# Kernel tuning notes

Measured on AMD Instinct MI355X. Metric: run time of the kernel, lower is better.

Reference implementation:

```python
import jax, jax.numpy as jnp
import numpy as np

B = 32768
NPG = 15            # nodes per graph (5 segments * 3 nodes)
NSEG = 5
FEAT = 8
HID = 64
BIAS_SP = float(np.log(np.exp(1.0) - 1.0))  # biased_softplus_1.0 bias
SCALE_LB = 1e-4


def _edge_template():
    eg = []
    for s in range(NSEG):
        t = 3 * s
        eg += [(t, t + 1), (t + 1, t), (t, t + 2), (t + 2, t)]
    for s in range(NSEG - 1):
        eg += [(3 * s, 3 * s + 3), (3 * s + 3, 3 * s)]
    return np.asarray(eg, dtype=np.int64)  # [28, 2]


def setup_inputs() -> dict:
    key = jax.random.key(0)
    ks = jax.random.split(key, 16)
    N = B * NPG
    x = jax.random.normal(ks[0], (N, FEAT), dtype=jnp.float32)
    tmpl = _edge_template()
    offs = (np.arange(B, dtype=np.int64) * NPG)[:, None]          # [B,1]
    src = (tmpl[:, 0][None, :] + offs).ravel()
    dst = (tmpl[:, 1][None, :] + offs).ravel()
    edge_index = jnp.asarray(np.stack([src, dst]), dtype=jnp.int32)  # [2,E]
    sd = 0.05
    params = dict(
        Wt=jax.random.normal(ks[1], (FEAT, HID), jnp.float32) * sd,
        bt=jax.random.normal(ks[2], (HID,), jnp.float32) * sd,
        Wl=jax.random.normal(ks[3], (4, HID), jnp.float32) * sd,
        bl=jax.random.normal(ks[4], (HID,), jnp.float32) * sd,
        gc_Wroot=jax.random.normal(ks[5], (3, HID, HID), jnp.float32) * sd,
        gc_Wrel=jax.random.normal(ks[6], (3, HID, HID), jnp.float32) * sd,
        gc_b=jax.random.normal(ks[7], (3, HID), jnp.float32) * sd,
        leg_W=jax.random.normal(ks[8], (10, HID, 4), jnp.float32) * sd,
        leg_b=jax.random.normal(ks[9], (10, 4), jnp.float32) * sd,
        torso_W=jax.random.normal(ks[10], (4, HID, 4), jnp.float32) * sd,
        torso_b=jax.random.normal(ks[11], (4, 4), jnp.float32) * sd,
    )
    return dict(x=x, edge_index=edge_index, batch_size=B, **params)


def reference(x, edge_index, batch_size, Wt, bt, Wl, bl,
              gc_Wroot, gc_Wrel, gc_b, leg_W, leg_b, torso_W, torso_b):
    N = x.shape[0]
    npg = N // batch_size              # 15
    nseg = npg // 3                    # 5
    pos = jnp.arange(N) % npg
    is_torso = (pos % 3) == 0          # nodes 0,3,6,... within each graph

    # Per-type input encoders + tanh, merged by mask (original scatters into h)
    h_t = jnp.tanh(x @ Wt + bt)
    h_l = jnp.tanh(x[:, :4] @ Wl + bl)
    h = jnp.where(is_torso[:, None], h_t, h_l)        # [N, 64]

    src, dst = edge_index[0], edge_index[1]
    for i in range(3):
        agg = jax.ops.segment_sum(h[src], dst, num_segments=N)
        h = jnp.tanh(agg @ gc_Wrel[i] + gc_b[i] + h @ gc_Wroot[i])

    hp = h.reshape(batch_size, npg, HID)              # [B, 15, 64]

    leg_pos = jnp.array([p for p in range(1, npg) if p % 3 != 0])   # 10 legs
    torso_pos = jnp.array([3 * s for s in range(1, nseg)])          # 4 torsos

    leg_out = jnp.einsum('bnd,ndk->bnk', hp[:, leg_pos], leg_W) + leg_b      # [B,10,4]
    torso_out = jnp.einsum('bnd,ndk->bnk', hp[:, torso_pos], torso_W) + torso_b  # [B,4,4]

    # Blocks are emitted in node-position order 1..14 within each graph
    blocks = jnp.zeros((batch_size, npg - 1, 4), dtype=h.dtype)
    blocks = blocks.at[:, leg_pos - 1].set(leg_out)
    blocks = blocks.at[:, torso_pos - 1].set(torso_out)
    out = blocks.reshape(batch_size, 2 * (npg - 1), 2)               # [B,28,2]

    loc = out[..., 0]
    scale = jnp.maximum(jax.nn.softplus(out[..., 1] + BIAS_SP), SCALE_LB)
    return loc, scale
```

## Files before the change

### kernel.cpp

```cpp
#include <hip/hip_runtime.h>

#define NB 32768
#define GPB 8
#define THREADS 256
#define BIAS_SP 0.5413248546129181f

typedef __attribute__((ext_vector_type(8))) short bf16x8;
typedef __attribute__((ext_vector_type(4))) float f32x4;
typedef __attribute__((ext_vector_type(4))) unsigned int u32x4;

static __device__ __forceinline__ unsigned f2bfu(float f) {
    union { float f; unsigned u; } v; v.f = f;
    return (v.u + 0x8000u) >> 16;
}
static __device__ __forceinline__ float lof(unsigned u) {
    union { unsigned u; float f; } v; v.u = u << 16; return v.f;
}
static __device__ __forceinline__ float hif(unsigned u) {
    union { unsigned u; float f; } v; v.u = u & 0xFFFF0000u; return v.f;
}
static __device__ __forceinline__ float fast_tanh(float xx) {
    float e = __expf(2.0f * xx);
    return 1.0f - 2.0f * __builtin_amdgcn_rcpf(e + 1.0f);
}
#define CVTPK(d, a, b) asm("v_cvt_pk_bf16_f32 %0, %1, %2" : "=v"(d) : "v"(a), "v"(b))

__global__ void setup_kernel(const float* __restrict__ Wroot, const float* __restrict__ Wrel,
                             const float* __restrict__ legW, const float* __restrict__ torW,
                             const float* __restrict__ Wt, const float* __restrict__ bt,
                             const float* __restrict__ Wl, const float* __restrict__ bl,
                             unsigned* __restrict__ wsw) {
    const int t = blockIdx.x * 256 + threadIdx.x;
    if (t < 3072) {
        const int i = t >> 10, rem = t & 1023, s = rem >> 8, tt = rem & 255;
        const int lane = tt & 63, ctl = tt >> 6;
        const int bcol = (ctl << 4) + (lane & 15);
        const int kb = ((s & 1) << 5) + ((lane >> 4) << 3);
        const float* M = ((s < 2) ? Wroot : Wrel) + i * 4096 + kb * 64 + bcol;
        u32x4 d;
        #pragma unroll
        for (int dd = 0; dd < 4; ++dd)
            d[dd] = f2bfu(M[(2 * dd) * 64]) | (f2bfu(M[(2 * dd + 1) * 64]) << 16);
        *(u32x4*)(wsw + t * 4) = d;
    } else if (t < 3520) {
        const int t2 = t - 3072, item = t2 >> 3, k8 = t2 & 7;
        const int p = (item >> 2) + 1, j = item & 3;
        const int p3 = (p * 11) >> 5;
        const int pm3 = p - p3 * 3;
        const float* src;
        if (pm3 == 0) src = torW + (p3 - 1) * 256 + j;
        else          src = legW + (2 * p3 + pm3 - 1) * 256 + j;
        u32x4 d;
        #pragma unroll
        for (int dd = 0; dd < 4; ++dd) {
            const int k = (k8 << 3) + 2 * dd;
            d[dd] = f2bfu(src[k * 4]) | (f2bfu(src[(k + 1) * 4]) << 16);
        }
        *(u32x4*)(wsw + 12288 + t2 * 4) = d;
    } else if (t < 3776) {
        const int t3 = t - 3520;
        const int lane = t3 & 63, ctl = t3 >> 6;
        const int col = (ctl << 4) + (lane & 15);
        const int kg = lane >> 4;
        auto encval = [&](int k) -> float {
            if (k < 8)   return Wt[k * 64 + col];
            if (k < 12)  return Wl[(k - 8) * 64 + col];
            if (k == 12) return bt[col];
            if (k == 13) return bl[col];
            return 0.f;
        };
        u32x4 d;
        #pragma unroll
        for (int dd = 0; dd < 4; ++dd) {
            const int k0 = kg * 8 + 2 * dd;
            d[dd] = f2bfu(encval(k0)) | (f2bfu(encval(k0 + 1)) << 16);
        }
        *(u32x4*)(wsw + 14080 + t3 * 4) = d;
    }
}

__global__ __launch_bounds__(THREADS, 4) void leg_main(
    const float* __restrict__ x,
    const float* __restrict__ gcb,
    const float* __restrict__ legB, const float* __restrict__ torB,
    const unsigned* __restrict__ wsw,
    float* __restrict__ out)
{
    __shared__ __align__(16) unsigned char smem[GPB * 4096];
    const int tid  = threadIdx.x;
    const int lane = tid & 63;
    const int ct   = tid >> 6;
    const int g0   = blockIdx.x * GPB;

    const int bcol = (ct << 4) + (lane & 15);
    const float cb0 = gcb[bcol], cb1 = gcb[64 + bcol], cb2 = gcb[128 + bcol];

    const int row = lane & 15, kg = lane >> 4;
    const int row3 = (row * 11) >> 5;
    const int tors = row3 * 3;
    const int isT  = (row == tors);
    const int rowR = isT ? row : tors;
    const int voffA0  = row * 256 + (((kg ^ row) & 7) << 4);
    const int voffA1  = voffA0 ^ 0x40;
    const int voffA2  = rowR * 256 + (((kg ^ rowR) & 7) << 4) + (isT ? 128 : 0);
    const int voffA3  = voffA2 ^ 0x40;
    int voffC[4];
    #pragma unroll
    for (int r = 0; r < 4; ++r) {
        const int rr = (kg << 2) + r;
        voffC[r] = rr * 256 + (((((ct << 1) + ((lane >> 3) & 1)) ^ rr) & 7) << 4) + ((lane & 7) << 1);
    }

    const int c2 = lane & 31;
    unsigned char* gbase = smem + ((ct << 1) + (lane >> 5)) * 4096;
    const int aoff = (c2 & 3) << 2;
    int agg_ra[15];
    #pragma unroll
    for (int r = 0; r < 15; ++r)
        agg_ra[r] = r * 256 + ((((c2 >> 2) ^ r) & 7) << 4) + aoff;
    int agg_wa[5];
    #pragma unroll
    for (int i = 0; i < 5; ++i) {
        const int r = 3 * i;
        agg_wa[i] = r * 256 + 128 + ((((c2 >> 2) ^ r) & 7) << 4) + aoff;
    }
#define RD32(r)  (*(const unsigned*)(gbase + agg_ra[r]))
#define WR32(i, flo, fhi) do { unsigned _w; CVTPK(_w, flo, fhi); \
    *(unsigned*)(gbase + agg_wa[i]) = _w; } while (0)
#define AGG() do { \
    unsigned u[15]; \
    _Pragma("unroll") for (int r = 0; r < 15; ++r) u[r] = RD32(r); \
    float l3 = lof(u[3]), h3 = hif(u[3]), l6 = lof(u[6]), h6 = hif(u[6]), l9 = lof(u[9]), h9 = hif(u[9]); \
    WR32(0,  lof(u[1]) + lof(u[2]) + l3,              hif(u[1]) + hif(u[2]) + h3); \
    WR32(1,  lof(u[4]) + lof(u[5]) + lof(u[0]) + l6,  hif(u[4]) + hif(u[5]) + hif(u[0]) + h6); \
    WR32(2,  lof(u[7]) + lof(u[8]) + l3 + l9,         hif(u[7]) + hif(u[8]) + h3 + h9); \
    WR32(3,  lof(u[10]) + lof(u[11]) + l6 + lof(u[12]), hif(u[10]) + hif(u[11]) + h6 + hif(u[12])); \
    WR32(4,  lof(u[13]) + lof(u[14]) + l9,            hif(u[13]) + hif(u[14]) + h9); \
} while (0)
#define EPI() do { \
    _Pragma("unroll") for (int g = 0; g < GPB; ++g) { \
        _Pragma("unroll") for (int r = 0; r < 4; ++r) { \
            const float tv = fast_tanh(acc[g][r]); \
            unsigned uu; CVTPK(uu, tv, tv); \
            *(unsigned short*)(smem + g * 4096 + voffC[r]) = (unsigned short)uu; \
        } } } while (0)

    const unsigned mT = (isT && row < 15) ? 0xFFFFFFFFu : 0u;
    const unsigned mL = isT ? 0u : 0xFFFFFFFFu;
    const unsigned m01 = (kg == 0) ? mT : ((kg == 1) ? mL : 0u);
    const unsigned m45 = (kg == 0) ? mT : 0u;
    const unsigned c1213 = (kg == 1) ? ((mT ? 0x3F80u : 0u) | (mL ? 0x3F800000u : 0u)) : 0u;
    const int rowc = (row < 15) ? row : 0;
    const bf16x8 bfrE = *(const bf16x8*)(wsw + 14080 + tid * 4);

    f32x4 acc[GPB];
    #pragma unroll
    for (int g = 0; g < GPB; ++g) {
        const float4* xr = (const float4*)x + ((size_t)(g0 + g) * 15 + rowc) * 2;
        const float4 x0 = xr[0], x1 = xr[1];
        unsigned a01, a23, a45, a67;
        CVTPK(a01, x0.x, x0.y); CVTPK(a23, x0.z, x0.w);
        CVTPK(a45, x1.x, x1.y); CVTPK(a67, x1.z, x1.w);
        union { u32x4 u; bf16x8 b; } af;
        af.u[0] = a01 & m01;
        af.u[1] = a23 & m01;
        af.u[2] = (a45 & m45) | c1213;
        af.u[3] = a67 & m45;
        const f32x4 z = { 0.f, 0.f, 0.f, 0.f };
        acc[g] = __builtin_amdgcn_mfma_f32_16x16x32_bf16(af.b, bfrE, z, 0, 0, 0);
    }
    EPI();
    __syncthreads();
    AGG();
    __syncthreads();

    #pragma unroll
    for (int it = 0; it < 3; ++it) {
        bf16x8 bfr[4];
        #pragma unroll
        for (int s = 0; s < 4; ++s)
            bfr[s] = *(const bf16x8*)(wsw + ((it * 4 + s) * 256 + tid) * 4);
        const float cbi = (it == 0) ? cb0 : (it == 1) ? cb1 : cb2;
        #pragma unroll
        for (int g = 0; g < GPB; ++g) {
            const unsigned char* sg = smem + g * 4096;
            const bf16x8 a0 = *(const bf16x8*)(sg + voffA0);
            const bf16x8 a1 = *(const bf16x8*)(sg + voffA1);
            const bf16x8 a2 = *(const bf16x8*)(sg + voffA2);
            const bf16x8 a3 = *(const bf16x8*)(sg + voffA3);
            f32x4 c = { cbi, cbi, cbi, cbi };
            c = __builtin_amdgcn_mfma_f32_16x16x32_bf16(a0, bfr[0], c, 0, 0, 0);
            c = __builtin_amdgcn_mfma_f32_16x16x32_bf16(a1, bfr[1], c, 0, 0, 0);
            c = __builtin_amdgcn_mfma_f32_16x16x32_bf16(a2, bfr[2], c, 0, 0, 0);
            c = __builtin_amdgcn_mfma_f32_16x16x32_bf16(a3, bfr[3], c, 0, 0, 0);
            acc[g] = c;
        }
        __syncthreads();
        EPI();
        __syncthreads();
        if (it < 2) { AGG(); __syncthreads(); }
    }

    if (lane < 56) {
        const int p = (lane >> 2) + 1, j = lane & 3;
        const int p3 = (p * 11) >> 5;
        const int pm3 = p - p3 * 3;
        float bias;
        if (pm3 == 0) bias = torB[((p3 - 1) << 2) + j];
        else          bias = legB[(((p3 << 1) + pm3 - 1) << 2) + j];
        const unsigned* wp = wsw + 12288 + (lane << 5);
        const int ps = (p & 7) << 4;
        #pragma unroll
        for (int gs = 0; gs < 2; ++gs) {
            const int g = (ct << 1) + gs;
            const unsigned char* hb = smem + g * 4096 + p * 256;
            float acch = 0.f;
            #pragma unroll
            for (int k8 = 0; k8 < 8; ++k8) {
                const u32x4 hv = *(const u32x4*)(hb + (ps ^ (k8 << 4)));
                const u32x4 wv = *(const u32x4*)(wp + (k8 << 2));
                #pragma unroll
                for (int dd = 0; dd < 4; ++dd) {
                    acch = __builtin_fmaf(lof(hv[dd]), lof(wv[dd]), acch);
                    acch = __builtin_fmaf(hif(hv[dd]), hif(wv[dd]), acch);
                }
            }
            acch += bias;
            const int mloc = ((p - 1) << 1) + (j >> 1);
            const size_t ob = (size_t)(g0 + g) * 28 + mloc;
            if ((j & 1) == 0) {
                out[ob] = acch;
            } else {
                const float z = acch + BIAS_SP;
                const float sp = (z > 15.f) ? z : __logf(1.f + __expf(z));
                out[(size_t)NB * 28 + ob] = fmaxf(sp, 1e-4f);
            }
        }
    }
}

extern "C" void kernel_launch(void* const* d_in, const int* in_sizes, int n_in,
                              void* d_out, int out_size, void* d_ws, size_t ws_size,
                              hipStream_t stream) {
    (void)in_sizes; (void)n_in; (void)out_size; (void)ws_size;
    const float* x     = (const float*)d_in[0];
    const float* Wt    = (const float*)d_in[3];
    const float* bt    = (const float*)d_in[4];
    const float* Wl    = (const float*)d_in[5];
    const float* bl    = (const float*)d_in[6];
    const float* Wroot = (const float*)d_in[7];
    const float* Wrel  = (const float*)d_in[8];
    const float* gcb   = (const float*)d_in[9];
    const float* legW  = (const float*)d_in[10];
    const float* legB  = (const float*)d_in[11];
    const float* torW  = (const float*)d_in[12];
    const float* torB  = (const float*)d_in[13];
    unsigned* wsw = (unsigned*)d_ws;
    setup_kernel<<<15, 256, 0, stream>>>(Wroot, Wrel, legW, torW, Wt, bt, Wl, bl, wsw);
    leg_main<<<NB / GPB, 256, 0, stream>>>(x, gcb, legB, torB, wsw, (float*)d_out);
}
```

Measured before the change: 78.73 us.

## Double block threads so each wave group handles half the graphs

The block grows to 512 threads (8 waves), and each set of four column waves now processes 4 of the 8 graphs instead of all 8. This halves per-thread accumulators and MFMA work and raises the number of waves resident per CU, aiming to hide latency better. Aggregation still runs only on the first four waves. The output head gives each wave one graph. The cost is more barrier participants and idle waves during aggregation.

```diff
diff --git a/kernel.cpp b/kernel.cpp
--- a/kernel.cpp
+++ b/kernel.cpp
@@ -2,7 +2,7 @@
 
 #define NB 32768
 #define GPB 8
-#define THREADS 256
+#define THREADS 512
 #define BIAS_SP 0.5413248546129181f
 
 typedef __attribute__((ext_vector_type(8))) short bf16x8;
@@ -79,7 +79,7 @@
     }
 }
 
-__global__ __launch_bounds__(THREADS, 4) void leg_main(
+__global__ __launch_bounds__(THREADS, 8) void leg_main(
     const float* __restrict__ x,
     const float* __restrict__ gcb,
     const float* __restrict__ legB, const float* __restrict__ torB,
@@ -89,7 +89,9 @@
     __shared__ __align__(16) unsigned char smem[GPB * 4096];
     const int tid  = threadIdx.x;
     const int lane = tid & 63;
-    const int ct   = tid >> 6;
+    const int w    = tid >> 6;
+    const int ct   = w & 3;
+    const int gh   = w >> 2;
     const int g0   = blockIdx.x * GPB;
 
     const int bcol = (ct << 4) + (lane & 15);
@@ -112,7 +114,7 @@
     }
 
     const int c2 = lane & 31;
-    unsigned char* gbase = smem + ((ct << 1) + (lane >> 5)) * 4096;
+    unsigned char* gbase = smem + (((w & 3) << 1) + (lane >> 5)) * 4096;
     const int aoff = (c2 & 3) << 2;
     int agg_ra[15];
     #pragma unroll
@@ -138,11 +140,12 @@
     WR32(4,  lof(u[13]) + lof(u[14]) + l9,            hif(u[13]) + hif(u[14]) + h9); \
 } while (0)
 #define EPI() do { \
-    _Pragma("unroll") for (int g = 0; g < GPB; ++g) { \
+    _Pragma("unroll") for (int g = 0; g < 4; ++g) { \
+        unsigned char* sc = smem + ((gh << 2) + g) * 4096; \
         _Pragma("unroll") for (int r = 0; r < 4; ++r) { \
             const float tv = fast_tanh(acc[g][r]); \
             unsigned uu; CVTPK(uu, tv, tv); \
-            *(unsigned short*)(smem + g * 4096 + voffC[r]) = (unsigned short)uu; \
+            *(unsigned short*)(sc + voffC[r]) = (unsigned short)uu; \
         } } } while (0)
 
     const unsigned mT = (isT && row < 15) ? 0xFFFFFFFFu : 0u;
@@ -151,12 +154,13 @@
     const unsigned m45 = (kg == 0) ? mT : 0u;
     const unsigned c1213 = (kg == 1) ? ((mT ? 0x3F80u : 0u) | (mL ? 0x3F800000u : 0u)) : 0u;
     const int rowc = (row < 15) ? row : 0;
-    const bf16x8 bfrE = *(const bf16x8*)(wsw + 14080 + tid * 4);
-
-    f32x4 acc[GPB];
-    #pragma unroll
-    for (int g = 0; g < GPB; ++g) {
-        const float4* xr = (const float4*)x + ((size_t)(g0 + g) * 15 + rowc) * 2;
+    const bf16x8 bfrE = *(const bf16x8*)(wsw + 14080 + ((ct << 6) + lane) * 4);
+
+    f32x4 acc[4];
+    #pragma unroll
+    for (int g = 0; g < 4; ++g) {
+        const int gg = (gh << 2) + g;
+        const float4* xr = (const float4*)x + ((size_t)(g0 + gg) * 15 + rowc) * 2;
         const float4 x0 = xr[0], x1 = xr[1];
         unsigned a01, a23, a45, a67;
         CVTPK(a01, x0.x, x0.y); CVTPK(a23, x0.z, x0.w);
@@ -171,7 +175,7 @@
     }
     EPI();
     __syncthreads();
-    AGG();
+    if (w < 4) AGG();
     __syncthreads();
 
     #pragma unroll
@@ -179,11 +183,11 @@
         bf16x8 bfr[4];
         #pragma unroll
         for (int s = 0; s < 4; ++s)
-            bfr[s] = *(const bf16x8*)(wsw + ((it * 4 + s) * 256 + tid) * 4);
+            bfr[s] = *(const bf16x8*)(wsw + ((it * 4 + s) * 256 + (ct << 6) + lane) * 4);
         const float cbi = (it == 0) ? cb0 : (it == 1) ? cb1 : cb2;
         #pragma unroll
-        for (int g = 0; g < GPB; ++g) {
-            const unsigned char* sg = smem + g * 4096;
+        for (int g = 0; g < 4; ++g) {
+            const unsigned char* sg = smem + ((gh << 2) + g) * 4096;
             const bf16x8 a0 = *(const bf16x8*)(sg + voffA0);
             const bf16x8 a1 = *(const bf16x8*)(sg + voffA1);
             const bf16x8 a2 = *(const bf16x8*)(sg + voffA2);
@@ -198,7 +202,7 @@
         __syncthreads();
         EPI();
         __syncthreads();
-        if (it < 2) { AGG(); __syncthreads(); }
+        if (it < 2) { if (w < 4) AGG(); __syncthreads(); }
     }
 
     if (lane < 56) {
@@ -210,31 +214,27 @@
         else          bias = legB[(((p3 << 1) + pm3 - 1) << 2) + j];
         const unsigned* wp = wsw + 12288 + (lane << 5);
         const int ps = (p & 7) << 4;
-        #pragma unroll
-        for (int gs = 0; gs < 2; ++gs) {
-            const int g = (ct << 1) + gs;
-            const unsigned char* hb = smem + g * 4096 + p * 256;
-            float acch = 0.f;
+        const unsigned char* hb = smem + w * 4096 + p * 256;
+        float acch = 0.f;
+        #pragma unroll
+        for (int k8 = 0; k8 < 8; ++k8) {
+            const u32x4 hv = *(const u32x4*)(hb + (ps ^ (k8 << 4)));
+            const u32x4 wv = *(const u32x4*)(wp + (k8 << 2));
             #pragma unroll
-            for (int k8 = 0; k8 < 8; ++k8) {
-                const u32x4 hv = *(const u32x4*)(hb + (ps ^ (k8 << 4)));
-                const u32x4 wv = *(const u32x4*)(wp + (k8 << 2));
-                #pragma unroll
-                for (int dd = 0; dd < 4; ++dd) {
-                    acch = __builtin_fmaf(lof(hv[dd]), lof(wv[dd]), acch);
-                    acch = __builtin_fmaf(hif(hv[dd]), hif(wv[dd]), acch);
-                }
+            for (int dd = 0; dd < 4; ++dd) {
+                acch = __builtin_fmaf(lof(hv[dd]), lof(wv[dd]), acch);
+                acch = __builtin_fmaf(hif(hv[dd]), hif(wv[dd]), acch);
             }
-            acch += bias;
-            const int mloc = ((p - 1) << 1) + (j >> 1);
-            const size_t ob = (size_t)(g0 + g) * 28 + mloc;
-            if ((j & 1) == 0) {
-                out[ob] = acch;
-            } else {
-                const float z = acch + BIAS_SP;
-                const float sp = (z > 15.f) ? z : __logf(1.f + __expf(z));
-                out[(size_t)NB * 28 + ob] = fmaxf(sp, 1e-4f);
-            }
+        }
+        acch += bias;
+        const int mloc = ((p - 1) << 1) + (j >> 1);
+        const size_t ob = (size_t)(g0 + w) * 28 + mloc;
+        if ((j & 1) == 0) {
+            out[ob] = acch;
+        } else {
+            const float z = acch + BIAS_SP;
+            const float sp = (z > 15.f) ? z : __logf(1.f + __expf(z));
+            out[(size_t)NB * 28 + ob] = fmaxf(sp, 1e-4f);
         }
     }
 }
@@ -257,5 +257,5 @@
     const float* torB  = (const float*)d_in[13];
     unsigned* wsw = (unsigned*)d_ws;
     setup_kernel<<<15, 256, 0, stream>>>(Wroot, Wrel, legW, torW, Wt, bt, Wl, bl, wsw);
-    leg_main<<<NB / GPB, 256, 0, stream>>>(x, gcb, legB, torB, wsw, (float*)d_out);
-}
+    leg_main<<<NB / GPB, THREADS, 0, stream>>>(x, gcb, legB, torB, wsw, (float*)d_out);
+}
```

New measurement: 109.4 us. +39.0%, slower.

## Give each wavefront its own graph and drop block-wide barriers

Applied to the files above, without the earlier changes.

Work is repartitioned so each wavefront owns one whole graph and computes all four 16-column tiles itself, instead of each wave covering one column tile across eight graphs. Because each wave now only touches its own shared-memory region, the block-wide barriers become lgkmcnt waits, and shared memory per block drops to 16KB with 4 graphs per block. The cost is that every wave reloads all GraphConv weight fragments from global memory (16 bf16x8 loads per layer instead of 4), which adds L1/L2 traffic. Memory latency is also exposed more, since each wave has only one graph's worth of independent MFMA chains.

```diff
diff --git a/kernel.cpp b/kernel.cpp
--- a/kernel.cpp
+++ b/kernel.cpp
@@ -1,7 +1,6 @@
 #include <hip/hip_runtime.h>
 
 #define NB 32768
-#define GPB 8
 #define THREADS 256
 #define BIAS_SP 0.5413248546129181f
 
@@ -24,6 +23,7 @@
     return 1.0f - 2.0f * __builtin_amdgcn_rcpf(e + 1.0f);
 }
 #define CVTPK(d, a, b) asm("v_cvt_pk_bf16_f32 %0, %1, %2" : "=v"(d) : "v"(a), "v"(b))
+#define LWAIT() asm volatile("s_waitcnt lgkmcnt(0)" ::: "memory")
 
 __global__ void setup_kernel(const float* __restrict__ Wroot, const float* __restrict__ Wrel,
                              const float* __restrict__ legW, const float* __restrict__ torW,
@@ -86,14 +86,12 @@
     const unsigned* __restrict__ wsw,
     float* __restrict__ out)
 {
-    __shared__ __align__(16) unsigned char smem[GPB * 4096];
+    __shared__ __align__(16) unsigned char smem[4 * 4096];
     const int tid  = threadIdx.x;
     const int lane = tid & 63;
-    const int ct   = tid >> 6;
-    const int g0   = blockIdx.x * GPB;
-
-    const int bcol = (ct << 4) + (lane & 15);
-    const float cb0 = gcb[bcol], cb1 = gcb[64 + bcol], cb2 = gcb[128 + bcol];
+    const int w    = tid >> 6;
+    const int g    = blockIdx.x * 4 + w;
+    unsigned char* ME = smem + w * 4096;
 
     const int row = lane & 15, kg = lane >> 4;
     const int row3 = (row * 11) >> 5;
@@ -104,45 +102,45 @@
     const int voffA1  = voffA0 ^ 0x40;
     const int voffA2  = rowR * 256 + (((kg ^ rowR) & 7) << 4) + (isT ? 128 : 0);
     const int voffA3  = voffA2 ^ 0x40;
-    int voffC[4];
+    int voffC0[4];
     #pragma unroll
     for (int r = 0; r < 4; ++r) {
         const int rr = (kg << 2) + r;
-        voffC[r] = rr * 256 + (((((ct << 1) + ((lane >> 3) & 1)) ^ rr) & 7) << 4) + ((lane & 7) << 1);
-    }
-
-    const int c2 = lane & 31;
-    unsigned char* gbase = smem + ((ct << 1) + (lane >> 5)) * 4096;
-    const int aoff = (c2 & 3) << 2;
-    int agg_ra[15];
+        voffC0[r] = rr * 256 + (((((lane >> 3) & 1) ^ rr) & 7) << 4) + ((lane & 7) << 1);
+    }
+
+    float cbv[3][4];
     #pragma unroll
-    for (int r = 0; r < 15; ++r)
-        agg_ra[r] = r * 256 + ((((c2 >> 2) ^ r) & 7) << 4) + aoff;
-    int agg_wa[5];
-    #pragma unroll
-    for (int i = 0; i < 5; ++i) {
-        const int r = 3 * i;
-        agg_wa[i] = r * 256 + 128 + ((((c2 >> 2) ^ r) & 7) << 4) + aoff;
-    }
-#define RD32(r)  (*(const unsigned*)(gbase + agg_ra[r]))
-#define WR32(i, flo, fhi) do { unsigned _w; CVTPK(_w, flo, fhi); \
-    *(unsigned*)(gbase + agg_wa[i]) = _w; } while (0)
+    for (int it = 0; it < 3; ++it)
+        #pragma unroll
+        for (int c = 0; c < 4; ++c)
+            cbv[it][c] = gcb[it * 64 + (c << 4) + (lane & 15)];
+
+    const int d = lane & 31, half = lane >> 5;
+    const int Abase = ((d >> 2) << 4) | ((d & 3) << 2);
+#define RDg(r)  (*(const unsigned*)(ME + (r) * 256 + (Abase ^ (((r) & 7) << 4))))
+#define WRg(r, flo, fhi) do { unsigned _w; CVTPK(_w, flo, fhi); \
+    *(unsigned*)(ME + (r) * 256 + 128 + (Abase ^ (((r) & 7) << 4))) = _w; } while (0)
 #define AGG() do { \
-    unsigned u[15]; \
-    _Pragma("unroll") for (int r = 0; r < 15; ++r) u[r] = RD32(r); \
-    float l3 = lof(u[3]), h3 = hif(u[3]), l6 = lof(u[6]), h6 = hif(u[6]), l9 = lof(u[9]), h9 = hif(u[9]); \
-    WR32(0,  lof(u[1]) + lof(u[2]) + l3,              hif(u[1]) + hif(u[2]) + h3); \
-    WR32(1,  lof(u[4]) + lof(u[5]) + lof(u[0]) + l6,  hif(u[4]) + hif(u[5]) + hif(u[0]) + h6); \
-    WR32(2,  lof(u[7]) + lof(u[8]) + l3 + l9,         hif(u[7]) + hif(u[8]) + h3 + h9); \
-    WR32(3,  lof(u[10]) + lof(u[11]) + l6 + lof(u[12]), hif(u[10]) + hif(u[11]) + h6 + hif(u[12])); \
-    WR32(4,  lof(u[13]) + lof(u[14]) + l9,            hif(u[13]) + hif(u[14]) + h9); \
+    if (half == 0) { \
+        const unsigned u0 = RDg(0), u1 = RDg(1), u2 = RDg(2), u3 = RDg(3), u4 = RDg(4); \
+        const unsigned u5 = RDg(5), u6 = RDg(6), u7 = RDg(7), u8 = RDg(8), u9 = RDg(9); \
+        WRg(0, lof(u1) + lof(u2) + lof(u3),            hif(u1) + hif(u2) + hif(u3)); \
+        WRg(3, lof(u4) + lof(u5) + lof(u0) + lof(u6),  hif(u4) + hif(u5) + hif(u0) + hif(u6)); \
+        WRg(6, lof(u7) + lof(u8) + lof(u3) + lof(u9),  hif(u7) + hif(u8) + hif(u3) + hif(u9)); \
+    } else { \
+        const unsigned u6 = RDg(6), u9 = RDg(9), u10 = RDg(10), u11 = RDg(11); \
+        const unsigned u12 = RDg(12), u13 = RDg(13), u14 = RDg(14); \
+        WRg(9,  lof(u10) + lof(u11) + lof(u6) + lof(u12), hif(u10) + hif(u11) + hif(u6) + hif(u12)); \
+        WRg(12, lof(u13) + lof(u14) + lof(u9),            hif(u13) + hif(u14) + hif(u9)); \
+    } \
 } while (0)
 #define EPI() do { \
-    _Pragma("unroll") for (int g = 0; g < GPB; ++g) { \
+    _Pragma("unroll") for (int c = 0; c < 4; ++c) { \
         _Pragma("unroll") for (int r = 0; r < 4; ++r) { \
-            const float tv = fast_tanh(acc[g][r]); \
+            const float tv = fast_tanh(acc[c][r]); \
             unsigned uu; CVTPK(uu, tv, tv); \
-            *(unsigned short*)(smem + g * 4096 + voffC[r]) = (unsigned short)uu; \
+            *(unsigned short*)(ME + (voffC0[r] ^ (c << 5))) = (unsigned short)uu; \
         } } } while (0)
 
     const unsigned mT = (isT && row < 15) ? 0xFFFFFFFFu : 0u;
@@ -151,12 +149,10 @@
     const unsigned m45 = (kg == 0) ? mT : 0u;
     const unsigned c1213 = (kg == 1) ? ((mT ? 0x3F80u : 0u) | (mL ? 0x3F800000u : 0u)) : 0u;
     const int rowc = (row < 15) ? row : 0;
-    const bf16x8 bfrE = *(const bf16x8*)(wsw + 14080 + tid * 4);
-
-    f32x4 acc[GPB];
-    #pragma unroll
-    for (int g = 0; g < GPB; ++g) {
-        const float4* xr = (const float4*)x + ((size_t)(g0 + g) * 15 + rowc) * 2;
+
+    f32x4 acc[4];
+    {
+        const float4* xr = (const float4*)x + ((size_t)g * 15 + rowc) * 2;
         const float4 x0 = xr[0], x1 = xr[1];
         unsigned a01, a23, a45, a67;
         CVTPK(a01, x0.x, x0.y); CVTPK(a23, x0.z, x0.w);
@@ -167,38 +163,45 @@
         af.u[2] = (a45 & m45) | c1213;
         af.u[3] = a67 & m45;
         const f32x4 z = { 0.f, 0.f, 0.f, 0.f };
-        acc[g] = __builtin_amdgcn_mfma_f32_16x16x32_bf16(af.b, bfrE, z, 0, 0, 0);
+        #pragma unroll
+        for (int c = 0; c < 4; ++c) {
+            const bf16x8 bfrE = *(const bf16x8*)(wsw + 14080 + (((c << 6) + lane) << 2));
+            acc[c] = __builtin_amdgcn_mfma_f32_16x16x32_bf16(af.b, bfrE, z, 0, 0, 0);
+        }
     }
     EPI();
-    __syncthreads();
+    LWAIT();
     AGG();
-    __syncthreads();
+    LWAIT();
 
     #pragma unroll
     for (int it = 0; it < 3; ++it) {
-        bf16x8 bfr[4];
-        #pragma unroll
-        for (int s = 0; s < 4; ++s)
-            bfr[s] = *(const bf16x8*)(wsw + ((it * 4 + s) * 256 + tid) * 4);
-        const float cbi = (it == 0) ? cb0 : (it == 1) ? cb1 : cb2;
-        #pragma unroll
-        for (int g = 0; g < GPB; ++g) {
-            const unsigned char* sg = smem + g * 4096;
-            const bf16x8 a0 = *(const bf16x8*)(sg + voffA0);
-            const bf16x8 a1 = *(const bf16x8*)(sg + voffA1);
-            const bf16x8 a2 = *(const bf16x8*)(sg + voffA2);
-            const bf16x8 a3 = *(const bf16x8*)(sg + voffA3);
-            f32x4 c = { cbi, cbi, cbi, cbi };
-            c = __builtin_amdgcn_mfma_f32_16x16x32_bf16(a0, bfr[0], c, 0, 0, 0);
-            c = __builtin_amdgcn_mfma_f32_16x16x32_bf16(a1, bfr[1], c, 0, 0, 0);
-            c = __builtin_amdgcn_mfma_f32_16x16x32_bf16(a2, bfr[2], c, 0, 0, 0);
-            c = __builtin_amdgcn_mfma_f32_16x16x32_bf16(a3, bfr[3], c, 0, 0, 0);
-            acc[g] = c;
-        }
-        __syncthreads();
+        const bf16x8 a0 = *(const bf16x8*)(ME + voffA0);
+        const bf16x8 a1 = *(const bf16x8*)(ME + voffA1);
+        const bf16x8 a2 = *(const bf16x8*)(ME + voffA2);
+        const bf16x8 a3 = *(const bf16x8*)(ME + voffA3);
+        LWAIT();
+        #pragma unroll
+        for (int c = 0; c < 4; ++c) {
+            const unsigned* bp = wsw + (((it * 4) * 256 + (c << 6) + lane) << 2);
+            const bf16x8 b0 = *(const bf16x8*)(bp);
+            const bf16x8 b1 = *(const bf16x8*)(bp + 1024);
+            const bf16x8 b2 = *(const bf16x8*)(bp + 2048);
+            const bf16x8 b3 = *(const bf16x8*)(bp + 3072);
+            const float cbi = cbv[it][c];
+            f32x4 cc = { cbi, cbi, cbi, cbi };
+            cc = __builtin_amdgcn_mfma_f32_16x16x32_bf16(a0, b0, cc, 0, 0, 0);
+            cc = __builtin_amdgcn_mfma_f32_16x16x32_bf16(a1, b1, cc, 0, 0, 0);
+            cc = __builtin_amdgcn_mfma_f32_16x16x32_bf16(a2, b2, cc, 0, 0, 0);
+            cc = __builtin_amdgcn_mfma_f32_16x16x32_bf16(a3, b3, cc, 0, 0, 0);
+            acc[c] = cc;
+        }
         EPI();
-        __syncthreads();
-        if (it < 2) { AGG(); __syncthreads(); }
+        LWAIT();
+        if (it < 2) {
+            AGG();
+            LWAIT();
+        }
     }
 
     if (lane < 56) {
@@ -210,31 +213,27 @@
         else          bias = legB[(((p3 << 1) + pm3 - 1) << 2) + j];
         const unsigned* wp = wsw + 12288 + (lane << 5);
         const int ps = (p & 7) << 4;
-        #pragma unroll
-        for (int gs = 0; gs < 2; ++gs) {
-            const int g = (ct << 1) + gs;
-            const unsigned char* hb = smem + g * 4096 + p * 256;
-            float acch = 0.f;
+        const unsigned char* hb = ME + p * 256;
+        float acch = 0.f;
+        #pragma unroll
+        for (int k8 = 0; k8 < 8; ++k8) {
+            const u32x4 hv = *(const u32x4*)(hb + (ps ^ (k8 << 4)));
+            const u32x4 wv = *(const u32x4*)(wp + (k8 << 2));
             #pragma unroll
-            for (int k8 = 0; k8 < 8; ++k8) {
-                const u32x4 hv = *(const u32x4*)(hb + (ps ^ (k8 << 4)));
-                const u32x4 wv = *(const u32x4*)(wp + (k8 << 2));
-                #pragma unroll
-                for (int dd = 0; dd < 4; ++dd) {
-                    acch = __builtin_fmaf(lof(hv[dd]), lof(wv[dd]), acch);
-                    acch = __builtin_fmaf(hif(hv[dd]), hif(wv[dd]), acch);
-                }
+            for (int dd = 0; dd < 4; ++dd) {
+                acch = __builtin_fmaf(lof(hv[dd]), lof(wv[dd]), acch);
+                acch = __builtin_fmaf(hif(hv[dd]), hif(wv[dd]), acch);
             }
-            acch += bias;
-            const int mloc = ((p - 1) << 1) + (j >> 1);
-            const size_t ob = (size_t)(g0 + g) * 28 + mloc;
-            if ((j & 1) == 0) {
-                out[ob] = acch;
-            } else {
-                const float z = acch + BIAS_SP;
-                const float sp = (z > 15.f) ? z : __logf(1.f + __expf(z));
-                out[(size_t)NB * 28 + ob] = fmaxf(sp, 1e-4f);
-            }
+        }
+        acch += bias;
+        const int mloc = ((p - 1) << 1) + (j >> 1);
+        const size_t ob = (size_t)g * 28 + mloc;
+        if ((j & 1) == 0) {
+            out[ob] = acch;
+        } else {
+            const float z = acch + BIAS_SP;
+            const float sp = (z > 15.f) ? z : __logf(1.f + __expf(z));
+            out[(size_t)NB * 28 + ob] = fmaxf(sp, 1e-4f);
         }
     }
 }
@@ -257,5 +256,5 @@
     const float* torB  = (const float*)d_in[13];
     unsigned* wsw = (unsigned*)d_ws;
     setup_kernel<<<15, 256, 0, stream>>>(Wroot, Wrel, legW, torW, Wt, bt, Wl, bl, wsw);
-    leg_main<<<NB / GPB, 256, 0, stream>>>(x, gcb, legB, torB, wsw, (float*)d_out);
-}
+    leg_main<<<NB / 4, THREADS, 0, stream>>>(x, gcb, legB, torB, wsw, (float*)d_out);
+}
```

Measured after the change: 93.54 us. +18.8%, slower.

## Replace LDS neighbor aggregation with adjacency-matrix MFMA applied after Wrel projection

Applied to the files above, without the earlier changes.

Each GraphConv layer now relies on associativity: it computes h·Wrel first, then multiplies that result by a constant per-graph 15-node adjacency pattern on the matrix cores. This replaces the separate LDS gather-and-sum pass for the aggregated features. The aggregated half of the shared-memory tile and its extra barriers go away, halving LDS use per block. The cost is a fifth MFMA per graph and rounding the intermediate h·Wrel to bf16, which may shift numerical accuracy.

```diff
diff --git a/kernel.cpp b/kernel.cpp
--- a/kernel.cpp
+++ b/kernel.cpp
@@ -24,6 +24,11 @@
     return 1.0f - 2.0f * __builtin_amdgcn_rcpf(e + 1.0f);
 }
 #define CVTPK(d, a, b) asm("v_cvt_pk_bf16_f32 %0, %1, %2" : "=v"(d) : "v"(a), "v"(b))
+
+__constant__ unsigned short SMASK[16] = {
+    0x000E, 0x0001, 0x0001, 0x0071, 0x0008, 0x0008, 0x0388, 0x0040,
+    0x0040, 0x1C40, 0x0200, 0x0200, 0x6200, 0x1000, 0x1000, 0x0000
+};
 
 __global__ void setup_kernel(const float* __restrict__ Wroot, const float* __restrict__ Wrel,
                              const float* __restrict__ legW, const float* __restrict__ torW,
@@ -86,7 +91,7 @@
     const unsigned* __restrict__ wsw,
     float* __restrict__ out)
 {
-    __shared__ __align__(16) unsigned char smem[GPB * 4096];
+    __shared__ __align__(16) unsigned char smem[GPB * 2048];
     const int tid  = threadIdx.x;
     const int lane = tid & 63;
     const int ct   = tid >> 6;
@@ -96,57 +101,33 @@
     const float cb0 = gcb[bcol], cb1 = gcb[64 + bcol], cb2 = gcb[128 + bcol];
 
     const int row = lane & 15, kg = lane >> 4;
-    const int row3 = (row * 11) >> 5;
-    const int tors = row3 * 3;
-    const int isT  = (row == tors);
-    const int rowR = isT ? row : tors;
-    const int voffA0  = row * 256 + (((kg ^ row) & 7) << 4);
-    const int voffA1  = voffA0 ^ 0x40;
-    const int voffA2  = rowR * 256 + (((kg ^ rowR) & 7) << 4) + (isT ? 128 : 0);
-    const int voffA3  = voffA2 ^ 0x40;
+    const int voffA0 = row * 128 + (((kg ^ row) & 7) << 4);
+    const int voffA1 = voffA0 ^ 0x40;
     int voffC[4];
     #pragma unroll
     for (int r = 0; r < 4; ++r) {
         const int rr = (kg << 2) + r;
-        voffC[r] = rr * 256 + (((((ct << 1) + ((lane >> 3) & 1)) ^ rr) & 7) << 4) + ((lane & 7) << 1);
-    }
-
-    const int c2 = lane & 31;
-    unsigned char* gbase = smem + ((ct << 1) + (lane >> 5)) * 4096;
-    const int aoff = (c2 & 3) << 2;
-    int agg_ra[15];
-    #pragma unroll
-    for (int r = 0; r < 15; ++r)
-        agg_ra[r] = r * 256 + ((((c2 >> 2) ^ r) & 7) << 4) + aoff;
-    int agg_wa[5];
-    #pragma unroll
-    for (int i = 0; i < 5; ++i) {
-        const int r = 3 * i;
-        agg_wa[i] = r * 256 + 128 + ((((c2 >> 2) ^ r) & 7) << 4) + aoff;
-    }
-#define RD32(r)  (*(const unsigned*)(gbase + agg_ra[r]))
-#define WR32(i, flo, fhi) do { unsigned _w; CVTPK(_w, flo, fhi); \
-    *(unsigned*)(gbase + agg_wa[i]) = _w; } while (0)
-#define AGG() do { \
-    unsigned u[15]; \
-    _Pragma("unroll") for (int r = 0; r < 15; ++r) u[r] = RD32(r); \
-    float l3 = lof(u[3]), h3 = hif(u[3]), l6 = lof(u[6]), h6 = hif(u[6]), l9 = lof(u[9]), h9 = hif(u[9]); \
-    WR32(0,  lof(u[1]) + lof(u[2]) + l3,              hif(u[1]) + hif(u[2]) + h3); \
-    WR32(1,  lof(u[4]) + lof(u[5]) + lof(u[0]) + l6,  hif(u[4]) + hif(u[5]) + hif(u[0]) + h6); \
-    WR32(2,  lof(u[7]) + lof(u[8]) + l3 + l9,         hif(u[7]) + hif(u[8]) + h3 + h9); \
-    WR32(3,  lof(u[10]) + lof(u[11]) + l6 + lof(u[12]), hif(u[10]) + hif(u[11]) + h6 + hif(u[12])); \
-    WR32(4,  lof(u[13]) + lof(u[14]) + l9,            hif(u[13]) + hif(u[14]) + h9); \
-} while (0)
+        voffC[r] = rr * 128 + (((((ct << 1) + ((lane >> 3) & 1)) ^ rr) & 7) << 4) + ((lane & 7) << 1);
+    }
+
+    const unsigned sm = SMASK[row];
+    union { u32x4 u; bf16x8 b; } sf;
+    #pragma unroll
+    for (int j2 = 0; j2 < 4; ++j2)
+        sf.u[j2] = ((sm >> ((kg << 2) + j2)) & 1) ? 0x3F80u : 0u;
+
 #define EPI() do { \
     _Pragma("unroll") for (int g = 0; g < GPB; ++g) { \
         _Pragma("unroll") for (int r = 0; r < 4; ++r) { \
             const float tv = fast_tanh(acc[g][r]); \
             unsigned uu; CVTPK(uu, tv, tv); \
-            *(unsigned short*)(smem + g * 4096 + voffC[r]) = (unsigned short)uu; \
+            *(unsigned short*)(smem + g * 2048 + voffC[r]) = (unsigned short)uu; \
         } } } while (0)
 
-    const unsigned mT = (isT && row < 15) ? 0xFFFFFFFFu : 0u;
-    const unsigned mL = isT ? 0u : 0xFFFFFFFFu;
+    const int nmod3 = row - ((row * 11) >> 5) * 3;
+    const bool nT = (nmod3 == 0);
+    const unsigned mT = (nT && row < 15) ? 0xFFFFFFFFu : 0u;
+    const unsigned mL = nT ? 0u : 0xFFFFFFFFu;
     const unsigned m01 = (kg == 0) ? mT : ((kg == 1) ? mL : 0u);
     const unsigned m45 = (kg == 0) ? mT : 0u;
     const unsigned c1213 = (kg == 1) ? ((mT ? 0x3F80u : 0u) | (mL ? 0x3F800000u : 0u)) : 0u;
@@ -171,8 +152,6 @@
     }
     EPI();
     __syncthreads();
-    AGG();
-    __syncthreads();
 
     #pragma unroll
     for (int it = 0; it < 3; ++it) {
@@ -183,22 +162,26 @@
         const float cbi = (it == 0) ? cb0 : (it == 1) ? cb1 : cb2;
         #pragma unroll
         for (int g = 0; g < GPB; ++g) {
-            const unsigned char* sg = smem + g * 4096;
+            const unsigned char* sg = smem + g * 2048;
             const bf16x8 a0 = *(const bf16x8*)(sg + voffA0);
             const bf16x8 a1 = *(const bf16x8*)(sg + voffA1);
-            const bf16x8 a2 = *(const bf16x8*)(sg + voffA2);
-            const bf16x8 a3 = *(const bf16x8*)(sg + voffA3);
-            f32x4 c = { cbi, cbi, cbi, cbi };
-            c = __builtin_amdgcn_mfma_f32_16x16x32_bf16(a0, bfr[0], c, 0, 0, 0);
-            c = __builtin_amdgcn_mfma_f32_16x16x32_bf16(a1, bfr[1], c, 0, 0, 0);
-            c = __builtin_amdgcn_mfma_f32_16x16x32_bf16(a2, bfr[2], c, 0, 0, 0);
-            c = __builtin_amdgcn_mfma_f32_16x16x32_bf16(a3, bfr[3], c, 0, 0, 0);
-            acc[g] = c;
+            f32x4 V = { cbi, cbi, cbi, cbi };
+            V = __builtin_amdgcn_mfma_f32_16x16x32_bf16(a0, bfr[0], V, 0, 0, 0);
+            V = __builtin_amdgcn_mfma_f32_16x16x32_bf16(a1, bfr[1], V, 0, 0, 0);
+            const f32x4 z = { 0.f, 0.f, 0.f, 0.f };
+            f32x4 U;
+            U = __builtin_amdgcn_mfma_f32_16x16x32_bf16(a0, bfr[2], z, 0, 0, 0);
+            U = __builtin_amdgcn_mfma_f32_16x16x32_bf16(a1, bfr[3], U, 0, 0, 0);
+            union { u32x4 u; bf16x8 b; } ub;
+            ub.u[0] = f2bfu(U[0]);
+            ub.u[1] = f2bfu(U[1]);
+            ub.u[2] = f2bfu(U[2]);
+            ub.u[3] = f2bfu(U[3]);
+            acc[g] = __builtin_amdgcn_mfma_f32_16x16x32_bf16(sf.b, ub.b, V, 0, 0, 0);
         }
         __syncthreads();
         EPI();
         __syncthreads();
-        if (it < 2) { AGG(); __syncthreads(); }
     }
 
     if (lane < 56) {
@@ -213,7 +196,7 @@
         #pragma unroll
         for (int gs = 0; gs < 2; ++gs) {
             const int g = (ct << 1) + gs;
-            const unsigned char* hb = smem + g * 4096 + p * 256;
+            const unsigned char* hb = smem + g * 2048 + p * 128;
             float acch = 0.f;
             #pragma unroll
             for (int k8 = 0; k8 < 8; ++k8) {
@@ -257,5 +240,5 @@
     const float* torB  = (const float*)d_in[13];
     unsigned* wsw = (unsigned*)d_ws;
     setup_kernel<<<15, 256, 0, stream>>>(Wroot, Wrel, legW, torW, Wt, bt, Wl, bl, wsw);
-    leg_main<<<NB / GPB, 256, 0, stream>>>(x, gcb, legB, torB, wsw, (float*)d_out);
-}
+    leg_main<<<NB / GPB, THREADS, 0, stream>>>(x, gcb, legB, torB, wsw, (float*)d_out);
+}
```

Result: faster. 76.75 us, median of 2 (-2.5%).
